# Kernel optimization log

Measured on AMD Instinct MI355X. Metric: run time of the kernel, lower is better.

Reference implementation:

```python
import jax, jax.numpy as jnp
import numpy as np
from jax import lax

C = 256
POOL = 7
NUM_CLASSES = 81
D = NUM_CLASSES - 1
STRIDES = (4, 8, 16, 32)
DEC_MULT = (0.1, 0.1, 0.2, 0.2)  # decode_settings: multipliers on raw deltas
LOG_MAX = float(np.log(1000.0 / 16.0))


def setup_inputs() -> dict:
    key = jax.random.key(0)
    ks = jax.random.split(key, 16)
    n, Rp = 2, 512
    R = n * Rp
    img = 800.0
    cx = jax.random.uniform(ks[0], (R,), minval=0.0, maxval=img)
    cy = jax.random.uniform(ks[1], (R,), minval=0.0, maxval=img)
    w = jax.random.uniform(ks[2], (R,), minval=16.0, maxval=300.0)
    h = jax.random.uniform(ks[3], (R,), minval=16.0, maxval=300.0)
    x1 = jnp.clip(cx - w / 2, 0.0, img - 1.0)
    y1 = jnp.clip(cy - h / 2, 0.0, img - 1.0)
    x2 = jnp.minimum(jnp.maximum(cx + w / 2, x1 + 1.0), img)
    y2 = jnp.minimum(jnp.maximum(cy + h / 2, y1 + 1.0), img)
    proposals = jnp.stack([x1, y1, x2, y2], -1)
    imidx = jnp.repeat(jnp.arange(n, dtype=jnp.int32), Rp)
    fmaps = {}
    for li, s in enumerate(STRIDES):
        hw = int(800 // s)
        fmaps[f"fmap{li}"] = jax.random.normal(ks[4 + li], (n, hw, hw, C), jnp.float32)
    c1, clin = C * POOL * POOL, 1024
    def lin(k, fi, fo):
        return (jax.random.normal(k, (fi, fo), jnp.float32) / np.sqrt(fi).astype(np.float32),
                jnp.zeros((fo,), jnp.float32))
    W0, b0 = lin(ks[8], c1, clin)
    W1, b1 = lin(ks[9], clin, clin)
    Wc, bc = lin(ks[10], clin, NUM_CLASSES)
    Wr, br = lin(ks[11], clin, NUM_CLASSES * 4)
    imsizes = jnp.full((n, 2), img, jnp.float32)  # (h, w) per image
    return dict(proposals=proposals, imidx=imidx, **fmaps,
                W0=W0, b0=b0, W1=W1, b1=b1, Wc=Wc, bc=bc, Wr=Wr, br=br,
                imsizes=imsizes, score_thr=0.05, iou_thr=0.5, imtop=100, min_size=1.0)


def _roi_align_level(fmap, boxes, imidx, stride):
    # fmap [n,H,W,C], boxes [R,4] xyxy in image coords; 1 sample per bin, bilinear.
    n, H, W, c = fmap.shape
    s = 1.0 / stride
    x1, y1, x2, y2 = boxes[:, 0] * s, boxes[:, 1] * s, boxes[:, 2] * s, boxes[:, 3] * s
    g = (jnp.arange(POOL, dtype=jnp.float32) + 0.5) / POOL  # bin centers in [0,1]
    xs = x1[:, None] + g[None, :] * (x2 - x1)[:, None] - 0.5  # [R,POOL]
    ys = y1[:, None] + g[None, :] * (y2 - y1)[:, None] - 0.5
    R = boxes.shape[0]
    xx = jnp.broadcast_to(xs[:, None, :], (R, POOL, POOL))
    yy = jnp.broadcast_to(ys[:, :, None], (R, POOL, POOL))
    x0f, y0f = jnp.floor(xx), jnp.floor(yy)
    wx, wy = xx - x0f, yy - y0f
    x0 = jnp.clip(x0f.astype(jnp.int32), 0, W - 1)
    x1i = jnp.clip(x0f.astype(jnp.int32) + 1, 0, W - 1)
    y0 = jnp.clip(y0f.astype(jnp.int32), 0, H - 1)
    y1i = jnp.clip(y0f.astype(jnp.int32) + 1, 0, H - 1)
    ii = imidx[:, None, None]
    v00 = fmap[ii, y0, x0]; v01 = fmap[ii, y0, x1i]
    v10 = fmap[ii, y1i, x0]; v11 = fmap[ii, y1i, x1i]  # each [R,POOL,POOL,C]
    wx, wy = wx[..., None], wy[..., None]
    return (v00 * (1 - wx) * (1 - wy) + v01 * wx * (1 - wy)
            + v10 * (1 - wx) * wy + v11 * wx * wy)


def _forward(proposals, imidx, fmaps, W0, b0, W1, b1, Wc, bc, Wr, br,
             imsizes, score_thr, iou_thr, imtop, min_size):
    R = proposals.shape[0]
    pw = proposals[:, 2] - proposals[:, 0]
    ph = proposals[:, 3] - proposals[:, 1]
    # FPN level assignment (torchvision canonical formula)
    lvl = jnp.floor(4.0 + jnp.log2(jnp.sqrt(pw * ph) / 224.0 + 1e-6))
    lvl = jnp.clip(lvl, 2, 5).astype(jnp.int32) - 2
    pooled = jnp.zeros((R, POOL, POOL, C), fmaps[0].dtype)
    for k, (fm, st) in enumerate(zip(fmaps, STRIDES)):
        pk = _roi_align_level(fm, proposals, imidx, st)
        pooled = jnp.where((lvl == k)[:, None, None, None], pk, pooled)
    # two-FC head + cls/reg
    x = pooled.reshape(R, -1)
    x = jax.nn.relu(x @ W0 + b0)
    x = jax.nn.relu(x @ W1 + b1)
    reg = (x @ Wr + br).reshape(R, NUM_CLASSES, 4)[:, 1:]      # [R,D,4]
    scr = jax.nn.softmax(x @ Wc + bc, axis=-1)[:, 1:]          # [R,D]
    cls = jnp.broadcast_to(jnp.arange(1, NUM_CLASSES, dtype=jnp.int32), (R, D))
    # decode boxes (proposal cwh + weighted deltas, log-space clamp)
    cx = (proposals[:, 0] + proposals[:, 2]) * 0.5
    cy = (proposals[:, 1] + proposals[:, 3]) * 0.5
    dx = reg[..., 0] * DEC_MULT[0]
    dy = reg[..., 1] * DEC_MULT[1]
    dw = jnp.minimum(reg[..., 2] * DEC_MULT[2], LOG_MAX)
    dh = jnp.minimum(reg[..., 3] * DEC_MULT[3], LOG_MAX)
    ncx = dx * pw[:, None] + cx[:, None]
    ncy = dy * ph[:, None] + cy[:, None]
    nw = jnp.exp(dw) * pw[:, None]
    nh = jnp.exp(dh) * ph[:, None]
    hb = imsizes[imidx, 0][:, None]
    wb = imsizes[imidx, 1][:, None]
    bx1 = jnp.clip(ncx - nw / 2, 0.0, wb); bx2 = jnp.clip(ncx + nw / 2, 0.0, wb)
    by1 = jnp.clip(ncy - nh / 2, 0.0, hb); by2 = jnp.clip(ncy + nh / 2, 0.0, hb)
    boxes = jnp.stack([bx1, by1, bx2, by2], -1)                # [R,D,4]
    valid = (scr > score_thr) & (bx2 - bx1 >= min_size) & (by2 - by1 >= min_size)
    # flatten roi-class pairs; class-offset boxes = torchvision batched_nms trick
    M = R * D
    boxes_f = boxes.reshape(M, 4)
    scr_f = scr.reshape(M)
    cls_f = cls.reshape(M)
    valid_f = valid.reshape(M)
    imidx_f = jnp.repeat(imidx, D)
    off = cls_f.astype(boxes_f.dtype)[:, None] * (jnp.max(imsizes) + 2.0)
    bo = boxes_f + off
    areas = (bo[:, 2] - bo[:, 0]) * (bo[:, 3] - bo[:, 1])
    def nms(scores0):
        def step(scores, _):
            i = jnp.argmax(scores)
            s = scores[i]
            b = bo[i]
            iw = jnp.clip(jnp.minimum(b[2], bo[:, 2]) - jnp.maximum(b[0], bo[:, 0]), 0.0)
            ih = jnp.clip(jnp.minimum(b[3], bo[:, 3]) - jnp.maximum(b[1], bo[:, 1]), 0.0)
            inter = iw * ih
            iou = inter / (areas[i] + areas - inter + 1e-6)
            scores = jnp.where(iou > iou_thr, -1.0, scores)
            scores = scores.at[i].set(-1.0)
            return scores, (i, s)
        _, (idx, s) = lax.scan(step, scores0, None, length=imtop)
        return idx, s
    n = imsizes.shape[0]
    ob, osc, ocl = [], [], []
    for i in range(n):
        s0 = jnp.where(valid_f & (imidx_f == i), scr_f, -1.0)
        idx, s = nms(s0)
        keep = s > 0.0  # padded slots have score <= 0
        ob.append(jnp.where(keep[:, None], boxes_f[idx], 0.0))
        osc.append(jnp.where(keep, s, 0.0))
        ocl.append(jnp.where(keep, cls_f[idx], -1))
    return jnp.stack(ob), jnp.stack(osc), jnp.stack(ocl)


def reference(proposals, imidx, fmap0, fmap1, fmap2, fmap3, W0, b0, W1, b1,
              Wc, bc, Wr, br, imsizes, score_thr, iou_thr, imtop, min_size):
    return _forward(proposals, imidx, (fmap0, fmap1, fmap2, fmap3), W0, b0, W1,
                    b1, Wc, bc, Wr, br, imsizes, score_thr, iou_thr, int(imtop),
                    min_size)
```

## Files before the change

kernel.cpp:

```cpp
#include <hip/hip_runtime.h>
#include <math.h>

#define CCH 256
#define NPOOL 7
#define NCLS 81
#define DCLS 80
#define NHEAD 512
#define FLOG_MAX 4.1351666f

typedef _Float16 half8 __attribute__((ext_vector_type(8)));
typedef _Float16 half4 __attribute__((ext_vector_type(4)));
typedef float floatx4 __attribute__((ext_vector_type(4)));

__global__ void zero_k(float4* __restrict__ p, int count4)
{
    int i = blockIdx.x * blockDim.x + threadIdx.x;
    if (i < count4) p[i] = make_float4(0.f, 0.f, 0.f, 0.f);
}

__device__ __forceinline__ void roi_setup(
    const float* __restrict__ prop, const int* __restrict__ imidx,
    const float* __restrict__ f0, const float* __restrict__ f1,
    const float* __restrict__ f2, const float* __restrict__ f3,
    int h0, int h1, int h2, int h3, int b,
// ... 173 lines not shown
                            const float* __restrict__ bias,
                            _Float16* __restrict__ outH,
                            _Float16* __restrict__ outL,
                            int total, int CL)
{
    int i = (blockIdx.x * blockDim.x + threadIdx.x) * 4;
    if (i >= total) return;
    int b = i % CL;
    float4 v = *(const float4*)(acc + i);
    float4 bb = *(const float4*)(bias + b);
    const float* pv = (const float*)&v;
    const float* pb = (const float*)&bb;
    half4 h, l;
#pragma unroll
    for (int e = 0; e < 4; ++e) {
        float f = fmaxf(pv[e] + pb[e], 0.0f);
        _Float16 hh = (_Float16)f;
        h[e] = hh;
        l[e] = (_Float16)(f - (float)hh);
    }
    *(half4*)(outH + i) = h;
    *(half4*)(outL + i) = l;
}

__device__ __forceinline__ void dma16(const _Float16* g, _Float16* l)
{
    __builtin_amdgcn_global_load_lds(
        (const __attribute__((address_space(1))) unsigned int*)g,
        (__attribute__((address_space(3))) unsigned int*)l, 16, 0, 0);
}

#define LDKE 32

__global__ __launch_bounds__(256) void gemm_mfma_split_k(
    const _Float16* __restrict__ Ah, const _Float16* __restrict__ Al,
    const _Float16* __restrict__ Bh, const _Float16* __restrict__ Bl,
    float* __restrict__ Cacc, int M, int N, int K, int Kc, int SP)
{
    __shared__ _Float16 sAh[128 * LDKE], sAl[128 * LDKE];
    __shared__ _Float16 sBh[128 * LDKE], sBl[128 * LDKE];

    int bid = blockIdx.x;
    int z = bid % SP;
    int q = bid / SP;
    int NT = N >> 7;
    int nn = q % NT;
    int m = q / NT;
    int m0 = m * 128, n0 = nn * 128;
    int kb = z * Kc;
    int ke = min(K, kb + Kc);

    int t = threadIdx.x;
    int lane = t & 63, w = t >> 6;
    int wr = w >> 1, wc = w & 1;
    int fr = lane & 15;
    int fk = (lane >> 4) * 8;

    int drow = w * 32 + (lane >> 2);
    int dkq = (lane & 3) * 8;
    const _Float16* gAh = Ah + (size_t)(m0 + drow) * K + dkq;
    const _Float16* gAl = Al + (size_t)(m0 + drow) * K + dkq;
    const _Float16* gBh = Bh + (size_t)(n0 + drow) * K + dkq;
    const _Float16* gBl = Bl + (size_t)(n0 + drow) * K + dkq;
    size_t rowskip = (size_t)16 * K;

    _Float16* lAh0 = &sAh[(w * 2 + 0) * 512];
    _Float16* lAh1 = &sAh[(w * 2 + 1) * 512];
    _Float16* lAl0 = &sAl[(w * 2 + 0) * 512];
    _Float16* lAl1 = &sAl[(w * 2 + 1) * 512];
    _Float16* lBh0 = &sBh[(w * 2 + 0) * 512];
    _Float16* lBh1 = &sBh[(w * 2 + 1) * 512];
    _Float16* lBl0 = &sBl[(w * 2 + 0) * 512];
    _Float16* lBl1 = &sBl[(w * 2 + 1) * 512];

    floatx4 acc[4][4] = {};

    for (int k0 = kb; k0 < ke; k0 += 32) {
        dma16(gAh + k0, lAh0);
        dma16(gAh + rowskip + k0, lAh1);
        dma16(gAl + k0, lAl0);
        dma16(gAl + rowskip + k0, lAl1);
        dma16(gBh + k0, lBh0);
        dma16(gBh + rowskip + k0, lBh1);
        dma16(gBl + k0, lBl0);
        dma16(gBl + rowskip + k0, lBl1);
        __syncthreads();

        half8 ah[4], al[4], bh[4], bl[4];
#pragma unroll
        for (int i = 0; i < 4; ++i) {
            int ar = wr * 64 + i * 16 + fr;
            ah[i] = *(const half8*)&sAh[ar * LDKE + fk];
            al[i] = *(const half8*)&sAl[ar * LDKE + fk];
            int bc = wc * 64 + i * 16 + fr;
            bh[i] = *(const half8*)&sBh[bc * LDKE + fk];
            bl[i] = *(const half8*)&sBl[bc * LDKE + fk];
        }
#pragma unroll
        for (int i = 0; i < 4; ++i)
#pragma unroll
            for (int j = 0; j < 4; ++j) {
                acc[i][j] = __builtin_amdgcn_mfma_f32_16x16x32_f16(ah[i], bh[j], acc[i][j], 0, 0, 0);
                acc[i][j] = __builtin_amdgcn_mfma_f32_16x16x32_f16(ah[i], bl[j], acc[i][j], 0, 0, 0);
                acc[i][j] = __builtin_amdgcn_mfma_f32_16x16x32_f16(al[i], bh[j], acc[i][j], 0, 0, 0);
            }
        __syncthreads();
    }

    int rbase = (lane >> 4) * 4;
#pragma unroll
    for (int i = 0; i < 4; ++i)
#pragma unroll
        for (int j = 0; j < 4; ++j) {
            int col = n0 + wc * 64 + j * 16 + fr;
#pragma unroll
            for (int r = 0; r < 4; ++r) {
                int row = m0 + wr * 64 + i * 16 + rbase + r;
                atomicAdd(&Cacc[(size_t)row * N + col], acc[i][j][r]);
            }
        }
}

__global__ __launch_bounds__(256) void gemm_mfma_fused64_k(
    const _Float16* __restrict__ Ah, const _Float16* __restrict__ Al,
    const _Float16* __restrict__ Bh, const _Float16* __restrict__ Bl,
    const float* __restrict__ bias,
    float* __restrict__ Cout,
    _Float16* __restrict__ outH, _Float16* __restrict__ outL,
    int M, int N, int K, int mode)
{
    __shared__ _Float16 sAh[64 * LDKE], sAl[64 * LDKE];
    __shared__ _Float16 sBh[64 * LDKE], sBl[64 * LDKE];

    int m0 = blockIdx.y * 64, n0 = blockIdx.x * 64;
    int t = threadIdx.x;
    int lane = t & 63, w = t >> 6;
    int wr = w >> 1, wc = w & 1;
    int fr = lane & 15;
    int fk = (lane >> 4) * 8;

    int drow = w * 16 + (lane >> 2);
    int dkq = (lane & 3) * 8;
    const _Float16* gAh = Ah + (size_t)(m0 + drow) * K + dkq;
    const _Float16* gAl = Al + (size_t)(m0 + drow) * K + dkq;
    const _Float16* gBh = Bh + (size_t)(n0 + drow) * K + dkq;
    const _Float16* gBl = Bl + (size_t)(n0 + drow) * K + dkq;
    _Float16* lAh = &sAh[w * 512];
    _Float16* lAl = &sAl[w * 512];
    _Float16* lBh = &sBh[w * 512];
    _Float16* lBl = &sBl[w * 512];

    floatx4 acc[2][2] = {};

    for (int k0 = 0; k0 < K; k0 += 32) {
        dma16(gAh + k0, lAh);
        dma16(gAl + k0, lAl);
        dma16(gBh + k0, lBh);
        dma16(gBl + k0, lBl);
        __syncthreads();

        half8 ah[2], av[2], bh[2], bv[2];
#pragma unroll
        for (int i = 0; i < 2; ++i) {
            int ar = wr * 32 + i * 16 + fr;
            ah[i] = *(const half8*)&sAh[ar * LDKE + fk];
            av[i] = *(const half8*)&sAl[ar * LDKE + fk];
            int bc = wc * 32 + i * 16 + fr;
            bh[i] = *(const half8*)&sBh[bc * LDKE + fk];
            bv[i] = *(const half8*)&sBl[bc * LDKE + fk];
        }
#pragma unroll
        for (int i = 0; i < 2; ++i)
#pragma unroll
            for (int j = 0; j < 2; ++j) {
                acc[i][j] = __builtin_amdgcn_mfma_f32_16x16x32_f16(ah[i], bh[j], acc[i][j], 0, 0, 0);
                acc[i][j] = __builtin_amdgcn_mfma_f32_16x16x32_f16(ah[i], bv[j], acc[i][j], 0, 0, 0);
                acc[i][j] = __builtin_amdgcn_mfma_f32_16x16x32_f16(av[i], bh[j], acc[i][j], 0, 0, 0);
            }
        __syncthreads();
    }

    int rbase = (lane >> 4) * 4;
#pragma unroll
    for (int i = 0; i < 2; ++i)
#pragma unroll
        for (int j = 0; j < 2; ++j) {
            int col = n0 + wc * 32 + j * 16 + fr;
#pragma unroll
            for (int r = 0; r < 4; ++r) {
                int row = m0 + wr * 32 + i * 16 + rbase + r;
                float v = acc[i][j][r];
                if (mode == 0) {
                    Cout[(size_t)row * N + col] = v;
                } else {
                    float f = fmaxf(v + bias[col], 0.0f);
                    _Float16 hh = (_Float16)f;
                    outH[(size_t)row * N + col] = hh;
                    outL[(size_t)row * N + col] = (_Float16)(f - (float)hh);
                }
            }
        }
}
// ... 71 lines not shown
            if (col < N) atomicAdd(&Cacc[(size_t)row * N + col], acc[i][j]);
        }
    }
}

__global__ void softmax_k(const float* __restrict__ logits, int ldl,
                          const float* __restrict__ bc,
                          float* __restrict__ scr)
{
    int r = blockIdx.x;
    int t = threadIdx.x;
    const float* row = logits + (size_t)r * ldl;

    float v0 = row[t] + bc[t];
    float v1 = (t + 64 < NCLS) ? (row[t + 64] + bc[t + 64]) : -INFINITY;
    float m = fmaxf(v0, v1);
#pragma unroll
    for (int o = 32; o > 0; o >>= 1) m = fmaxf(m, __shfl_down(m, o));
    m = __shfl(m, 0);

    float e0 = expf(v0 - m);
    float e1 = (t + 64 < NCLS) ? expf(v1 - m) : 0.0f;
    float sum = e0 + e1;
#pragma unroll
    for (int o = 32; o > 0; o >>= 1) sum += __shfl_down(sum, o);
    sum = __shfl(sum, 0);
    float inv = 1.0f / sum;

    if (t >= 1)        scr[(size_t)r * DCLS + (t - 1)]  = e0 * inv;
    if (t + 64 < NCLS) scr[(size_t)r * DCLS + (t + 63)] = e1 * inv;
}

#define NMS_T 1024
__global__ __launch_bounds__(NMS_T) void nms_k(
    const float* __restrict__ scr,
    const float* __restrict__ prop,
    const int* __restrict__ imidx,
    const float* __restrict__ head, int ldh, int regofs,
    const float* __restrict__ br,
    const float* __restrict__ imsz,
    const float* __restrict__ score_thr_p,
    const float* __restrict__ min_size_p,
    const float* __restrict__ iou_thr_p,
    int* __restrict__ cidx,
    float* __restrict__ cscore,
    float* __restrict__ cbo,
    float* __restrict__ cbox,
    float* __restrict__ carea,
    float* __restrict__ out,
    int M, int n, int imtop)
{
    int img = blockIdx.x;
    int t = threadIdx.x;
    const int T = NMS_T;

    __shared__ int cnt;
    __shared__ float rs[NMS_T];
    __shared__ int rg[NMS_T];
    __shared__ int rl[NMS_T];
    __shared__ float wb0, wb1, wb2, wb3, wa;

    if (t == 0) cnt = 0;
    __syncthreads();

    float score_thr = score_thr_p[0];
    float min_size  = min_size_p[0];
    float iou_thr   = iou_thr_p[0];
    float immax = imsz[0];
    for (int q = 1; q < 2 * n; ++q) immax = fmaxf(immax, imsz[q]);

    int base = img * M;
    for (int j = t; j < M; j += T) {
        int r = j / DCLS;
        if (imidx[r] != img) continue;
        float s = scr[j];
        if (s <= score_thr) continue;

        int cls = j - r * DCLS + 1;
        const float* pr = prop + (size_t)r * 4;
        float pw = pr[2] - pr[0], ph = pr[3] - pr[1];
        float cx = (pr[0] + pr[2]) * 0.5f, cy = (pr[1] + pr[3]) * 0.5f;
        const float* rg_ = head + (size_t)r * ldh + regofs + cls * 4;
        const float* bb = br + cls * 4;
        float dx = (rg_[0] + bb[0]) * 0.1f;
        float dy = (rg_[1] + bb[1]) * 0.1f;
        float dw = fminf((rg_[2] + bb[2]) * 0.2f, FLOG_MAX);
        float dh = fminf((rg_[3] + bb[3]) * 0.2f, FLOG_MAX);
        float ncx = dx * pw + cx;
        float ncy = dy * ph + cy;
        float nw = expf(dw) * pw;
        float nh = expf(dh) * ph;
        float hbound = imsz[img * 2 + 0];
        float wbound = imsz[img * 2 + 1];
        float bx1 = fminf(fmaxf(ncx - nw * 0.5f, 0.0f), wbound);
        float bx2 = fminf(fmaxf(ncx + nw * 0.5f, 0.0f), wbound);
        float by1 = fminf(fmaxf(ncy - nh * 0.5f, 0.0f), hbound);
        float by2 = fminf(fmaxf(ncy + nh * 0.5f, 0.0f), hbound);
        if (bx2 - bx1 < min_size || by2 - by1 < min_size) continue;

        float off = (float)cls * (immax + 2.0f);
        int p = atomicAdd(&cnt, 1);
        cidx[base + p] = j;
        cscore[base + p] = s;
        cbox[(size_t)(base + p) * 4 + 0] = bx1;
        cbox[(size_t)(base + p) * 4 + 1] = by1;
        cbox[(size_t)(base + p) * 4 + 2] = bx2;
        cbox[(size_t)(base + p) * 4 + 3] = by2;
        cbo[(size_t)(base + p) * 4 + 0] = bx1 + off;
        cbo[(size_t)(base + p) * 4 + 1] = by1 + off;
        cbo[(size_t)(base + p) * 4 + 2] = bx2 + off;
        cbo[(size_t)(base + p) * 4 + 3] = by2 + off;
        carea[base + p] = (bx2 - bx1) * (by2 - by1);
    }
    __syncthreads();
    int K = cnt;

    float* ob  = out;
    float* osc = out + (size_t)n * imtop * 4;
    float* ocl = out + (size_t)n * imtop * 5;

    int it = 0;
    for (; it < imtop; ++it) {
        float best = -1e30f; int bg = 0x7fffffff; int bl = -1;
        for (int p = t; p < K; p += T) {
            float sv = cscore[base + p];
            int g = cidx[base + p];
            if (sv > best || (sv == best && g < bg)) { best = sv; bg = g; bl = p; }
        }
        rs[t] = best; rg[t] = bg; rl[t] = bl;
        __syncthreads();
        for (int o = T / 2; o > 0; o >>= 1) {
            if (t < o) {
                if (rs[t + o] > rs[t] || (rs[t + o] == rs[t] && rg[t + o] < rg[t])) {
                    rs[t] = rs[t + o]; rg[t] = rg[t + o]; rl[t] = rl[t + o];
                }
            }
            __syncthreads();
        }
        float s = rs[0]; int g = rg[0]; int lp = rl[0];
        if (s <= 0.0f) break;

        if (t == 0) {
            size_t oslot = (size_t)img * imtop + it;
            ob[oslot * 4 + 0] = cbox[(size_t)(base + lp) * 4 + 0];
            ob[oslot * 4 + 1] = cbox[(size_t)(base + lp) * 4 + 1];
            ob[oslot * 4 + 2] = cbox[(size_t)(base + lp) * 4 + 2];
            ob[oslot * 4 + 3] = cbox[(size_t)(base + lp) * 4 + 3];
            osc[oslot] = s;
            ocl[oslot] = (float)(g % DCLS + 1);
            wb0 = cbo[(size_t)(base + lp) * 4 + 0];
            wb1 = cbo[(size_t)(base + lp) * 4 + 1];
            wb2 = cbo[(size_t)(base + lp) * 4 + 2];
            wb3 = cbo[(size_t)(base + lp) * 4 + 3];
            wa  = carea[base + lp];
            cscore[base + lp] = -1.0f;
        }
        __syncthreads();
        float b0 = wb0, b1 = wb1, b2 = wb2, b3 = wb3, ai = wa;
        for (int p = t; p < K; p += T) {
            float c0 = cbo[(size_t)(base + p) * 4 + 0];
            float c1 = cbo[(size_t)(base + p) * 4 + 1];
            float c2 = cbo[(size_t)(base + p) * 4 + 2];
            float c3 = cbo[(size_t)(base + p) * 4 + 3];
            float iw = fmaxf(fminf(b2, c2) - fmaxf(b0, c0), 0.0f);
            float ih = fmaxf(fminf(b3, c3) - fmaxf(b1, c1), 0.0f);
            float inter = iw * ih;
            float iou = inter / (ai + carea[base + p] - inter + 1e-6f);
            if (iou > iou_thr) cscore[base + p] = -1.0f;
        }
        __syncthreads();
    }

    for (int q = it + t; q < imtop; q += T) {
        size_t oslot = (size_t)img * imtop + q;
        ob[oslot * 4 + 0] = 0.0f;
        ob[oslot * 4 + 1] = 0.0f;
        ob[oslot * 4 + 2] = 0.0f;
        ob[oslot * 4 + 3] = 0.0f;
        osc[oslot] = 0.0f;
        ocl[oslot] = -1.0f;
    }
}

extern "C" void kernel_launch(void* const* d_in, const int* in_sizes, int n_in,
                              void* d_out, int out_size, void* d_ws, size_t ws_size,
                              hipStream_t stream)
{
    const float* prop   = (const float*)d_in[0];
    const int*   imidx  = (const int*)d_in[1];
    const float* f0     = (const float*)d_in[2];
    const float* f1     = (const float*)d_in[3];
    const float* f2     = (const float*)d_in[4];
    const float* f3     = (const float*)d_in[5];
    const float* W0     = (const float*)d_in[6];
    const float* b0     = (const float*)d_in[7];
    const float* W1     = (const float*)d_in[8];
    const float* b1     = (const float*)d_in[9];
    const float* Wc     = (const float*)d_in[10];
    const float* bc     = (const float*)d_in[11];
    const float* Wr     = (const float*)d_in[12];
    const float* br     = (const float*)d_in[13];
    const float* imsz   = (const float*)d_in[14];
    const float* sthr   = (const float*)d_in[15];
    const float* ithr   = (const float*)d_in[16];
    const float* msz    = (const float*)d_in[18];

    int R = in_sizes[1];
    int n = in_sizes[14] / 2;
    int imtop = out_size / (n * 6);
    int M = R * DCLS;
    int K0 = NPOOL * NPOOL * CCH;
    int CL = in_sizes[7];

    int h0 = (int)(sqrtf((float)(in_sizes[2] / (n * CCH))) + 0.5f);
    int h1 = (int)(sqrtf((float)(in_sizes[3] / (n * CCH))) + 0.5f);
    int h2 = (int)(sqrtf((float)(in_sizes[4] / (n * CCH))) + 0.5f);
    int h3 = (int)(sqrtf((float)(in_sizes[5] / (n * CCH))) + 0.5f);

    float* outf = (float*)d_out;

    size_t szPool  = (size_t)R * K0 * 2;
    size_t szX     = (size_t)R * CL * 4;
    size_t szHead  = (size_t)R * NHEAD * 4;
    size_t szWh    = (size_t)NHEAD * CL * 2;
    size_t szXh    = (size_t)R * CL * 2;
    size_t szW1t   = (size_t)CL * CL * 2;
    size_t szScr   = (size_t)R * DCLS * 4;

    size_t needed = 4 * szPool + 2 * szX + szHead + 2 * szWh
                  + 4 * szXh + 2 * szW1t + szScr;

    int splitK0 = 8;
    bool mfma_ok = (ws_size >= needed) && (R % 128 == 0) && (CL % 128 == 0)
                 && (K0 % (splitK0 * 32) == 0) && (CL % 32 == 0)
                 && ((R * 49) % 4 == 0);

    if (mfma_ok) {
        uint8_t* w = (uint8_t*)d_ws;
        size_t o = 0;
        _Float16* poolH   = (_Float16*)(w + o); o += szPool;
        _Float16* poolL   = (_Float16*)(w + o); o += szPool;
        _Float16* W0tH    = (_Float16*)(w + o); o += szPool;
        _Float16* W0tL    = (_Float16*)(w + o); o += szPool;
        float*    x0acc   = (float*)(w + o);    o += szX;
        float*    unused  = (float*)(w + o);    o += szX;
        float*    headacc = (float*)(w + o);    o += szHead;
        _Float16* WheadtH = (_Float16*)(w + o); o += szWh;
        _Float16* WheadtL = (_Float16*)(w + o); o += szWh;
        _Float16* x0H     = (_Float16*)(w + o); o += szXh;
        _Float16* x0L     = (_Float16*)(w + o); o += szXh;
        _Float16* x1H     = (_Float16*)(w + o); o += szXh;
        _Float16* x1L     = (_Float16*)(w + o); o += szXh;
        _Float16* W1tH    = (_Float16*)(w + o); o += szW1t;
        _Float16* W1tL    = (_Float16*)(w + o); o += szW1t;
        float*    scr     = (float*)(w + o);
        (void)unused;

        int*   cidx   = (int*)d_ws;
        float* cscore = (float*)(cidx + (size_t)n * M);
        float* cbo    = cscore + (size_t)n * M;
        float* cbox   = cbo + (size_t)n * M * 4;
        float* carea  = cbox + (size_t)n * M * 4;

        {
            int c4 = (int)(szX / 16);
            zero_k<<<dim3((c4 + 255) / 256), dim3(256), 0, stream>>>((float4*)x0acc, c4);
        }
        convert_w_t_k<<<dim3(K0 / 64, CL / 64), dim3(256), 0, stream>>>(W0, W0tH, W0tL, K0, CL);
        convert_w_t_k<<<dim3(CL / 64, CL / 64), dim3(256), 0, stream>>>(W1, W1tH, W1tL, CL, CL);
        convert_w_t_guard_k<<<dim3(CL / 64, (NCLS + 63) / 64), dim3(256), 0, stream>>>(
            Wc, WheadtH, WheadtL, CL, NCLS, CL, 0);
        convert_w_t_guard_k<<<dim3(CL / 64, (NCLS * 4 + 63) / 64), dim3(256), 0, stream>>>(
            Wr, WheadtH, WheadtL, CL, NCLS * 4, CL, NCLS);
        roi_align_f16v4_k<<<dim3(R * 49 / 4), dim3(256), 0, stream>>>(
            prop, imidx, f0, f1, f2, f3, h0, h1, h2, h3, poolH, poolL);
        gemm_mfma_split_k<<<dim3(splitK0 * (R / 128) * (CL / 128)), dim3(256), 0, stream>>>(
            poolH, poolL, W0tH, W0tL, x0acc, R, CL, K0, K0 / splitK0, splitK0);
        act_split_k<<<dim3((R * CL / 4 + 255) / 256), dim3(256), 0, stream>>>(
            x0acc, b0, x0H, x0L, R * CL, CL);
        gemm_mfma_fused64_k<<<dim3(CL / 64, R / 64), dim3(256), 0, stream>>>(
            x0H, x0L, W1tH, W1tL, b1, nullptr, x1H, x1L, R, CL, CL, 1);
        gemm_mfma_fused64_k<<<dim3(NHEAD / 64, R / 64), dim3(256), 0, stream>>>(
            x1H, x1L, WheadtH, WheadtL, nullptr, headacc, nullptr, nullptr, R, NHEAD, CL, 0);
        softmax_k<<<dim3(R), dim3(64), 0, stream>>>(headacc, NHEAD, bc, scr);
        nms_k<<<dim3(n), dim3(NMS_T), 0, stream>>>(
            scr, prop, imidx, headacc, NHEAD, NCLS, br, imsz, sthr, msz, ithr,
            cidx, cscore, cbo, cbox, carea, outf, M, n, imtop);
    } else {
        float* ws = (float*)d_ws;
        size_t off = 0;
        float* pooled  = ws + off; off += (size_t)R * K0;
        float* x0acc   = ws + off; off += (size_t)R * CL;
        float* x1acc   = ws + off; off += (size_t)R * CL;
        float* logits  = ws + off; off += (size_t)R * NCLS;
        off = (off + 3) & ~(size_t)3;
        float* reg     = ws + off; off += (size_t)R * NCLS * 4;
        float* scr     = ws + off; off += (size_t)R * DCLS;

        int*   cidx   = (int*)ws;
        float* cscore = (float*)(cidx + (size_t)n * M);
        float* cbo    = cscore + (size_t)n * M;
        float* cbox   = cbo + (size_t)n * M * 4;
        float* carea  = cbox + (size_t)n * M * 4;

        {
            size_t zcount = (size_t)(reg + (size_t)R * NCLS * 4 - x0acc);
            int c4 = (int)(zcount / 4);
            zero_k<<<dim3((c4 + 255) / 256), dim3(256), 0, stream>>>((float4*)x0acc, c4);
        }
        roi_align_k<<<dim3(R * 49), dim3(256), 0, stream>>>(
// ... 16 lines not shown
```

Measured before the change: 429.2 us.

## Use 256x256 double-buffered split-K GEMM with 512 threads and warp-shuffle NMS argmax

Replaces the 128x128 split-K fp16-split MFMA GEMM for the first FC layer with a 256x256 tile kernel using 8 waves and double-buffered LDS filled by global_load_lds. The A and B loads for the next k-step are interleaved between MFMA phases, with setprio and barriers. Split-K changes from 8 to 14. This aims to raise reuse per loaded byte and hide memory latency, at the cost of more registers (a 32-fragment accumulator), a large LDS footprint, and more atomics. The NMS argmax reduction is also moved from a shared-memory tree to warp shuffles, which cuts the number of barriers per iteration.

```diff
diff --git a/kernel.cpp b/kernel.cpp
--- a/kernel.cpp
+++ b/kernel.cpp
@@ -229,90 +229,183 @@
 
 #define LDKE 32
 
-__global__ __launch_bounds__(256) void gemm_mfma_split_k(
+__global__ __launch_bounds__(512, 2) void gemm_mfma_split256_k(
     const _Float16* __restrict__ Ah, const _Float16* __restrict__ Al,
     const _Float16* __restrict__ Bh, const _Float16* __restrict__ Bl,
     float* __restrict__ Cacc, int M, int N, int K, int Kc, int SP)
 {
-    __shared__ _Float16 sAh[128 * LDKE], sAl[128 * LDKE];
-    __shared__ _Float16 sBh[128 * LDKE], sBl[128 * LDKE];
+    __shared__ _Float16 lds[2][4][256 * LDKE];
 
     int bid = blockIdx.x;
-    int z = bid % SP;
-    int q = bid / SP;
-    int NT = N >> 7;
-    int nn = q % NT;
-    int m = q / NT;
-    int m0 = m * 128, n0 = nn * 128;
+    int MT = M >> 8, NT = N >> 8;
+    int tiles = MT * NT;
+    int z = bid / tiles;
+    int q = bid - z * tiles;
+    int nn = q % NT, mm = q / NT;
+    int m0 = mm << 8, n0 = nn << 8;
     int kb = z * Kc;
-    int ke = min(K, kb + Kc);
+    int nt = Kc >> 5;
 
     int t = threadIdx.x;
     int lane = t & 63, w = t >> 6;
-    int wr = w >> 1, wc = w & 1;
+    int wr = w >> 2, wc = w & 3;
     int fr = lane & 15;
     int fk = (lane >> 4) * 8;
 
-    int drow = w * 32 + (lane >> 2);
-    int dkq = (lane & 3) * 8;
-    const _Float16* gAh = Ah + (size_t)(m0 + drow) * K + dkq;
-    const _Float16* gAl = Al + (size_t)(m0 + drow) * K + dkq;
-    const _Float16* gBh = Bh + (size_t)(n0 + drow) * K + dkq;
-    const _Float16* gBl = Bl + (size_t)(n0 + drow) * K + dkq;
-    size_t rowskip = (size_t)16 * K;
-
-    _Float16* lAh0 = &sAh[(w * 2 + 0) * 512];
-    _Float16* lAh1 = &sAh[(w * 2 + 1) * 512];
-    _Float16* lAl0 = &sAl[(w * 2 + 0) * 512];
-    _Float16* lAl1 = &sAl[(w * 2 + 1) * 512];
-    _Float16* lBh0 = &sBh[(w * 2 + 0) * 512];
-    _Float16* lBh1 = &sBh[(w * 2 + 1) * 512];
-    _Float16* lBl0 = &sBl[(w * 2 + 0) * 512];
-    _Float16* lBl1 = &sBl[(w * 2 + 1) * 512];
-
-    floatx4 acc[4][4] = {};
-
-    for (int k0 = kb; k0 < ke; k0 += 32) {
-        dma16(gAh + k0, lAh0);
-        dma16(gAh + rowskip + k0, lAh1);
-        dma16(gAl + k0, lAl0);
-        dma16(gAl + rowskip + k0, lAl1);
-        dma16(gBh + k0, lBh0);
-        dma16(gBh + rowskip + k0, lBh1);
-        dma16(gBl + k0, lBl0);
-        dma16(gBl + rowskip + k0, lBl1);
-        __syncthreads();
-
-        half8 ah[4], al[4], bh[4], bl[4];
-#pragma unroll
-        for (int i = 0; i < 4; ++i) {
-            int ar = wr * 64 + i * 16 + fr;
-            ah[i] = *(const half8*)&sAh[ar * LDKE + fk];
-            al[i] = *(const half8*)&sAl[ar * LDKE + fk];
-            int bc = wc * 64 + i * 16 + fr;
-            bh[i] = *(const half8*)&sBh[bc * LDKE + fk];
-            bl[i] = *(const half8*)&sBl[bc * LDKE + fk];
-        }
-#pragma unroll
-        for (int i = 0; i < 4; ++i)
-#pragma unroll
-            for (int j = 0; j < 4; ++j) {
-                acc[i][j] = __builtin_amdgcn_mfma_f32_16x16x32_f16(ah[i], bh[j], acc[i][j], 0, 0, 0);
-                acc[i][j] = __builtin_amdgcn_mfma_f32_16x16x32_f16(ah[i], bl[j], acc[i][j], 0, 0, 0);
-                acc[i][j] = __builtin_amdgcn_mfma_f32_16x16x32_f16(al[i], bh[j], acc[i][j], 0, 0, 0);
-            }
-        __syncthreads();
-    }
+    int srow = t >> 2;
+    int sch = (t & 3) * 8;
+    const _Float16* gAh0 = Ah + (size_t)(m0 + srow) * K + sch;
+    const _Float16* gAl0 = Al + (size_t)(m0 + srow) * K + sch;
+    const _Float16* gBh0 = Bh + (size_t)(n0 + srow) * K + sch;
+    const _Float16* gBl0 = Bl + (size_t)(n0 + srow) * K + sch;
+    size_t rskip = (size_t)128 * K;
+    int d0 = t * 8;
+    int d1 = 4096 + t * 8;
+
+    floatx4 acc[8][4] = {};
+
+#define STAGE_A(b, kh) do { \
+    dma16(gAh0 + (kh), &lds[b][0][d0]); \
+    dma16(gAh0 + rskip + (kh), &lds[b][0][d1]); \
+    dma16(gAl0 + (kh), &lds[b][1][d0]); \
+    dma16(gAl0 + rskip + (kh), &lds[b][1][d1]); } while (0)
+#define STAGE_B(b, kh) do { \
+    dma16(gBh0 + (kh), &lds[b][2][d0]); \
+    dma16(gBh0 + rskip + (kh), &lds[b][2][d1]); \
+    dma16(gBl0 + (kh), &lds[b][3][d0]); \
+    dma16(gBl0 + rskip + (kh), &lds[b][3][d1]); } while (0)
+
+    STAGE_A(0, kb);
+    STAGE_B(0, kb);
+    asm volatile("s_waitcnt vmcnt(0)" ::: "memory");
+    __builtin_amdgcn_s_barrier();
+
+    int abase = wr * 128 + fr;
+    int bbase = wc * 64 + fr;
+
+#pragma unroll 1
+    for (int tt = 0; tt < nt; ++tt) {
+        int c = tt & 1, nb = c ^ 1;
+        bool hasnext = (tt + 1) < nt;
+        int kh = kb + (tt + 1) * 32;
+
+        const _Float16* sAh = lds[c][0];
+        const _Float16* sAl = lds[c][1];
+        const _Float16* sBh = lds[c][2];
+        const _Float16* sBl = lds[c][3];
+
+        half8 bhf[4], blf[4];
+        half8 a0h, a0l, a1h, a1l;
+
+#pragma unroll
+        for (int j = 0; j < 4; ++j) {
+            int bo = (bbase + j * 16) * LDKE + fk;
+            bhf[j] = *(const half8*)&sBh[bo];
+            blf[j] = *(const half8*)&sBl[bo];
+        }
+        {
+            int a0 = (abase + 0 * 16) * LDKE + fk;
+            int a1 = (abase + 1 * 16) * LDKE + fk;
+            a0h = *(const half8*)&sAh[a0]; a0l = *(const half8*)&sAl[a0];
+            a1h = *(const half8*)&sAh[a1]; a1l = *(const half8*)&sAl[a1];
+        }
+        if (hasnext) STAGE_A(nb, kh);
+        __builtin_amdgcn_s_barrier();
+        asm volatile("s_waitcnt lgkmcnt(0)" ::: "memory");
+        __builtin_amdgcn_sched_barrier(0);
+        __builtin_amdgcn_s_setprio(1);
+#pragma unroll
+        for (int j = 0; j < 4; ++j) {
+            acc[0][j] = __builtin_amdgcn_mfma_f32_16x16x32_f16(a0h, bhf[j], acc[0][j], 0, 0, 0);
+            acc[0][j] = __builtin_amdgcn_mfma_f32_16x16x32_f16(a0h, blf[j], acc[0][j], 0, 0, 0);
+            acc[0][j] = __builtin_amdgcn_mfma_f32_16x16x32_f16(a0l, bhf[j], acc[0][j], 0, 0, 0);
+            acc[1][j] = __builtin_amdgcn_mfma_f32_16x16x32_f16(a1h, bhf[j], acc[1][j], 0, 0, 0);
+            acc[1][j] = __builtin_amdgcn_mfma_f32_16x16x32_f16(a1h, blf[j], acc[1][j], 0, 0, 0);
+            acc[1][j] = __builtin_amdgcn_mfma_f32_16x16x32_f16(a1l, bhf[j], acc[1][j], 0, 0, 0);
+        }
+        __builtin_amdgcn_s_setprio(0);
+        __builtin_amdgcn_s_barrier();
+
+        {
+            int a0 = (abase + 2 * 16) * LDKE + fk;
+            int a1 = (abase + 3 * 16) * LDKE + fk;
+            a0h = *(const half8*)&sAh[a0]; a0l = *(const half8*)&sAl[a0];
+            a1h = *(const half8*)&sAh[a1]; a1l = *(const half8*)&sAl[a1];
+        }
+        if (hasnext) STAGE_B(nb, kh);
+        __builtin_amdgcn_s_barrier();
+        asm volatile("s_waitcnt lgkmcnt(0)" ::: "memory");
+        __builtin_amdgcn_sched_barrier(0);
+        __builtin_amdgcn_s_setprio(1);
+#pragma unroll
+        for (int j = 0; j < 4; ++j) {
+            acc[2][j] = __builtin_amdgcn_mfma_f32_16x16x32_f16(a0h, bhf[j], acc[2][j], 0, 0, 0);
+            acc[2][j] = __builtin_amdgcn_mfma_f32_16x16x32_f16(a0h, blf[j], acc[2][j], 0, 0, 0);
+            acc[2][j] = __builtin_amdgcn_mfma_f32_16x16x32_f16(a0l, bhf[j], acc[2][j], 0, 0, 0);
+            acc[3][j] = __builtin_amdgcn_mfma_f32_16x16x32_f16(a1h, bhf[j], acc[3][j], 0, 0, 0);
+            acc[3][j] = __builtin_amdgcn_mfma_f32_16x16x32_f16(a1h, blf[j], acc[3][j], 0, 0, 0);
+            acc[3][j] = __builtin_amdgcn_mfma_f32_16x16x32_f16(a1l, bhf[j], acc[3][j], 0, 0, 0);
+        }
+        __builtin_amdgcn_s_setprio(0);
+        __builtin_amdgcn_s_barrier();
+
+        {
+            int a0 = (abase + 4 * 16) * LDKE + fk;
+            int a1 = (abase + 5 * 16) * LDKE + fk;
+            a0h = *(const half8*)&sAh[a0]; a0l = *(const half8*)&sAl[a0];
+            a1h = *(const half8*)&sAh[a1]; a1l = *(const half8*)&sAl[a1];
+        }
+        __builtin_amdgcn_s_barrier();
+        asm volatile("s_waitcnt lgkmcnt(0)" ::: "memory");
+        __builtin_amdgcn_sched_barrier(0);
+        __builtin_amdgcn_s_setprio(1);
+#pragma unroll
+        for (int j = 0; j < 4; ++j) {
+            acc[4][j] = __builtin_amdgcn_mfma_f32_16x16x32_f16(a0h, bhf[j], acc[4][j], 0, 0, 0);
+            acc[4][j] = __builtin_amdgcn_mfma_f32_16x16x32_f16(a0h, blf[j], acc[4][j], 0, 0, 0);
+            acc[4][j] = __builtin_amdgcn_mfma_f32_16x16x32_f16(a0l, bhf[j], acc[4][j], 0, 0, 0);
+            acc[5][j] = __builtin_amdgcn_mfma_f32_16x16x32_f16(a1h, bhf[j], acc[5][j], 0, 0, 0);
+            acc[5][j] = __builtin_amdgcn_mfma_f32_16x16x32_f16(a1h, blf[j], acc[5][j], 0, 0, 0);
+            acc[5][j] = __builtin_amdgcn_mfma_f32_16x16x32_f16(a1l, bhf[j], acc[5][j], 0, 0, 0);
+        }
+        __builtin_amdgcn_s_setprio(0);
+        __builtin_amdgcn_s_barrier();
+
+        {
+            int a0 = (abase + 6 * 16) * LDKE + fk;
+            int a1 = (abase + 7 * 16) * LDKE + fk;
+            a0h = *(const half8*)&sAh[a0]; a0l = *(const half8*)&sAl[a0];
+            a1h = *(const half8*)&sAh[a1]; a1l = *(const half8*)&sAl[a1];
+        }
+        __builtin_amdgcn_s_barrier();
+        asm volatile("s_waitcnt lgkmcnt(0)" ::: "memory");
+        __builtin_amdgcn_sched_barrier(0);
+        __builtin_amdgcn_s_setprio(1);
+#pragma unroll
+        for (int j = 0; j < 4; ++j) {
+            acc[6][j] = __builtin_amdgcn_mfma_f32_16x16x32_f16(a0h, bhf[j], acc[6][j], 0, 0, 0);
+            acc[6][j] = __builtin_amdgcn_mfma_f32_16x16x32_f16(a0h, blf[j], acc[6][j], 0, 0, 0);
+            acc[6][j] = __builtin_amdgcn_mfma_f32_16x16x32_f16(a0l, bhf[j], acc[6][j], 0, 0, 0);
+            acc[7][j] = __builtin_amdgcn_mfma_f32_16x16x32_f16(a1h, bhf[j], acc[7][j], 0, 0, 0);
+            acc[7][j] = __builtin_amdgcn_mfma_f32_16x16x32_f16(a1h, blf[j], acc[7][j], 0, 0, 0);
+            acc[7][j] = __builtin_amdgcn_mfma_f32_16x16x32_f16(a1l, bhf[j], acc[7][j], 0, 0, 0);
+        }
+        __builtin_amdgcn_s_setprio(0);
+        asm volatile("s_waitcnt vmcnt(0)" ::: "memory");
+        __builtin_amdgcn_s_barrier();
+    }
+#undef STAGE_A
+#undef STAGE_B
 
     int rbase = (lane >> 4) * 4;
 #pragma unroll
-    for (int i = 0; i < 4; ++i)
+    for (int i = 0; i < 8; ++i)
 #pragma unroll
         for (int j = 0; j < 4; ++j) {
             int col = n0 + wc * 64 + j * 16 + fr;
 #pragma unroll
             for (int r = 0; r < 4; ++r) {
-                int row = m0 + wr * 64 + i * 16 + rbase + r;
+                int row = m0 + wr * 128 + i * 16 + rbase + r;
                 atomicAdd(&Cacc[(size_t)row * N + col], acc[i][j][r]);
             }
         }
@@ -523,11 +616,14 @@
     int img = blockIdx.x;
     int t = threadIdx.x;
     const int T = NMS_T;
+    const int NW = NMS_T / 64;
+    int lane = t & 63, wid = t >> 6;
 
     __shared__ int cnt;
-    __shared__ float rs[NMS_T];
-    __shared__ int rg[NMS_T];
-    __shared__ int rl[NMS_T];
+    __shared__ float wbs[NW];
+    __shared__ int wbg[NW];
+    __shared__ int wbl[NW];
+    __shared__ float fS;
     __shared__ float wb0, wb1, wb2, wb3, wa;
 
     if (t == 0) cnt = 0;
@@ -597,42 +693,56 @@
             int g = cidx[base + p];
             if (sv > best || (sv == best && g < bg)) { best = sv; bg = g; bl = p; }
         }
-        rs[t] = best; rg[t] = bg; rl[t] = bl;
+#pragma unroll
+        for (int o = 32; o > 0; o >>= 1) {
+            float os = __shfl_down(best, o);
+            int   og = __shfl_down(bg, o);
+            int   ol = __shfl_down(bl, o);
+            if (os > best || (os == best && og < bg)) { best = os; bg = og; bl = ol; }
+        }
+        if (lane == 0) { wbs[wid] = best; wbg[wid] = bg; wbl[wid] = bl; }
         __syncthreads();
-        for (int o = T / 2; o > 0; o >>= 1) {
-            if (t < o) {
-                if (rs[t + o] > rs[t] || (rs[t + o] == rs[t] && rg[t + o] < rg[t])) {
-                    rs[t] = rs[t + o]; rg[t] = rg[t + o]; rl[t] = rl[t + o];
+        if (wid == 0) {
+            float b2 = (lane < NW) ? wbs[lane] : -1e30f;
+            int   g2 = (lane < NW) ? wbg[lane] : 0x7fffffff;
+            int   l2 = (lane < NW) ? wbl[lane] : -1;
+#pragma unroll
+            for (int o = NW / 2; o > 0; o >>= 1) {
+                float os = __shfl_down(b2, o);
+                int   og = __shfl_down(g2, o);
+                int   ol = __shfl_down(l2, o);
+                if (os > b2 || (os == b2 && og < g2)) { b2 = os; g2 = og; l2 = ol; }
+            }
+            if (lane == 0) {
+                fS = b2;
+                if (b2 > 0.0f) {
+                    int lp = l2;
+                    size_t oslot = (size_t)img * imtop + it;
+                    ob[oslot * 4 + 0] = cbox[(size_t)(base + lp) * 4 + 0];
+                    ob[oslot * 4 + 1] = cbox[(size_t)(base + lp) * 4 + 1];
+                    ob[oslot * 4 + 2] = cbox[(size_t)(base + lp) * 4 + 2];
+                    ob[oslot * 4 + 3] = cbox[(size_t)(base + lp) * 4 + 3];
+                    osc[oslot] = b2;
+                    ocl[oslot] = (float)(g2 % DCLS + 1);
+                    wb0 = cbo[(size_t)(base + lp) * 4 + 0];
+                    wb1 = cbo[(size_t)(base + lp) * 4 + 1];
+                    wb2 = cbo[(size_t)(base + lp) * 4 + 2];
+                    wb3 = cbo[(size_t)(base + lp) * 4 + 3];
+                    wa  = carea[base + lp];
+                    cscore[base + lp] = -1.0f;
                 }
             }
-            __syncthreads();
-        }
-        float s = rs[0]; int g = rg[0]; int lp = rl[0];
-        if (s <= 0.0f) break;
-
-        if (t == 0) {
-            size_t oslot = (size_t)img * imtop + it;
-            ob[oslot * 4 + 0] = cbox[(size_t)(base + lp) * 4 + 0];
-            ob[oslot * 4 + 1] = cbox[(size_t)(base + lp) * 4 + 1];
-            ob[oslot * 4 + 2] = cbox[(size_t)(base + lp) * 4 + 2];
-            ob[oslot * 4 + 3] = cbox[(size_t)(base + lp) * 4 + 3];
-            osc[oslot] = s;
-            ocl[oslot] = (float)(g % DCLS + 1);
-            wb0 = cbo[(size_t)(base + lp) * 4 + 0];
-            wb1 = cbo[(size_t)(base + lp) * 4 + 1];
-            wb2 = cbo[(size_t)(base + lp) * 4 + 2];
-            wb3 = cbo[(size_t)(base + lp) * 4 + 3];
-            wa  = carea[base + lp];
-            cscore[base + lp] = -1.0f;
         }
         __syncthreads();
-        float b0 = wb0, b1 = wb1, b2 = wb2, b3 = wb3, ai = wa;
+        if (fS <= 0.0f) break;
+
+        float b0 = wb0, b1 = wb1, b2_ = wb2, b3 = wb3, ai = wa;
         for (int p = t; p < K; p += T) {
             float c0 = cbo[(size_t)(base + p) * 4 + 0];
             float c1 = cbo[(size_t)(base + p) * 4 + 1];
             float c2 = cbo[(size_t)(base + p) * 4 + 2];
             float c3 = cbo[(size_t)(base + p) * 4 + 3];
-            float iw = fmaxf(fminf(b2, c2) - fmaxf(b0, c0), 0.0f);
+            float iw = fmaxf(fminf(b2_, c2) - fmaxf(b0, c0), 0.0f);
             float ih = fmaxf(fminf(b3, c3) - fmaxf(b1, c1), 0.0f);
             float inter = iw * ih;
             float iou = inter / (ai + carea[base + p] - inter + 1e-6f);
@@ -700,10 +810,9 @@
     size_t needed = 4 * szPool + 2 * szX + szHead + 2 * szWh
                   + 4 * szXh + 2 * szW1t + szScr;
 
-    int splitK0 = 8;
-    bool mfma_ok = (ws_size >= needed) && (R % 128 == 0) && (CL % 128 == 0)
-                 && (K0 % (splitK0 * 32) == 0) && (CL % 32 == 0)
-                 && ((R * 49) % 4 == 0);
+    const int SP0 = 14;
+    bool mfma_ok = (ws_size >= needed) && (R % 256 == 0) && (CL % 256 == 0)
+                 && (K0 % (SP0 * 32) == 0) && ((R * 49) % 4 == 0);
 
     if (mfma_ok) {
         uint8_t* w = (uint8_t*)d_ws;
@@ -744,8 +853,8 @@
             Wr, WheadtH, WheadtL, CL, NCLS * 4, CL, NCLS);
         roi_align_f16v4_k<<<dim3(R * 49 / 4), dim3(256), 0, stream>>>(
             prop, imidx, f0, f1, f2, f3, h0, h1, h2, h3, poolH, poolL);
-        gemm_mfma_split_k<<<dim3(splitK0 * (R / 128) * (CL / 128)), dim3(256), 0, stream>>>(
-            poolH, poolL, W0tH, W0tL, x0acc, R, CL, K0, K0 / splitK0, splitK0);
+        gemm_mfma_split256_k<<<dim3(SP0 * (R / 256) * (CL / 256)), dim3(512), 0, stream>>>(
+            poolH, poolL, W0tH, W0tL, x0acc, R, CL, K0, K0 / SP0, SP0);
         act_split_k<<<dim3((R * CL / 4 + 255) / 256), dim3(256), 0, stream>>>(
             x0acc, b0, x0H, x0L, R * CL, CL);
         gemm_mfma_fused64_k<<<dim3(CL / 64, R / 64), dim3(256), 0, stream>>>(
```

New measurement: 449.4 us. 1.05x slower.

## Double-buffer fused64 GEMM LDS tiles and keep NMS candidates in registers

Applied to the files above, without the earlier changes.

The fused64 GEMM kernel now uses ping-pong shared-memory buffers and issues the DMA for the next K-tile before computing the current one, so global loads can overlap MFMA work. The NMS kernel replaces its 1024-wide shared-memory tree reduction with wave shuffles plus a small cross-wave step. When the candidate count fits, each thread holds up to 8 candidates' scores, boxes and areas in registers, which avoids re-reading global memory on every one of the up to 100 iterations. The cost is doubled LDS use in the GEMM and higher register pressure in NMS, which could lower occupancy.

```diff
diff --git a/kernel.cpp b/kernel.cpp
--- a/kernel.cpp
+++ b/kernel.cpp
@@ -326,8 +326,8 @@
     _Float16* __restrict__ outH, _Float16* __restrict__ outL,
     int M, int N, int K, int mode)
 {
-    __shared__ _Float16 sAh[64 * LDKE], sAl[64 * LDKE];
-    __shared__ _Float16 sBh[64 * LDKE], sBl[64 * LDKE];
+    __shared__ _Float16 sAh[2][64 * LDKE], sAl[2][64 * LDKE];
+    __shared__ _Float16 sBh[2][64 * LDKE], sBl[2][64 * LDKE];
 
     int m0 = blockIdx.y * 64, n0 = blockIdx.x * 64;
     int t = threadIdx.x;
@@ -342,29 +342,37 @@
     const _Float16* gAl = Al + (size_t)(m0 + drow) * K + dkq;
     const _Float16* gBh = Bh + (size_t)(n0 + drow) * K + dkq;
     const _Float16* gBl = Bl + (size_t)(n0 + drow) * K + dkq;
-    _Float16* lAh = &sAh[w * 512];
-    _Float16* lAl = &sAl[w * 512];
-    _Float16* lBh = &sBh[w * 512];
-    _Float16* lBl = &sBl[w * 512];
+    int lofs = w * 512;
+
+    int nt = K >> 5;
+
+    dma16(gAh + 0, &sAh[0][lofs]);
+    dma16(gAl + 0, &sAl[0][lofs]);
+    dma16(gBh + 0, &sBh[0][lofs]);
+    dma16(gBl + 0, &sBl[0][lofs]);
+    __syncthreads();
 
     floatx4 acc[2][2] = {};
 
-    for (int k0 = 0; k0 < K; k0 += 32) {
-        dma16(gAh + k0, lAh);
-        dma16(gAl + k0, lAl);
-        dma16(gBh + k0, lBh);
-        dma16(gBl + k0, lBl);
-        __syncthreads();
+    for (int tt = 0; tt < nt; ++tt) {
+        int c = tt & 1, nb = c ^ 1;
+        if (tt + 1 < nt) {
+            int k1 = (tt + 1) << 5;
+            dma16(gAh + k1, &sAh[nb][lofs]);
+            dma16(gAl + k1, &sAl[nb][lofs]);
+            dma16(gBh + k1, &sBh[nb][lofs]);
+            dma16(gBl + k1, &sBl[nb][lofs]);
+        }
 
         half8 ah[2], av[2], bh[2], bv[2];
 #pragma unroll
         for (int i = 0; i < 2; ++i) {
             int ar = wr * 32 + i * 16 + fr;
-            ah[i] = *(const half8*)&sAh[ar * LDKE + fk];
-            av[i] = *(const half8*)&sAl[ar * LDKE + fk];
+            ah[i] = *(const half8*)&sAh[c][ar * LDKE + fk];
+            av[i] = *(const half8*)&sAl[c][ar * LDKE + fk];
             int bc = wc * 32 + i * 16 + fr;
-            bh[i] = *(const half8*)&sBh[bc * LDKE + fk];
-            bv[i] = *(const half8*)&sBl[bc * LDKE + fk];
+            bh[i] = *(const half8*)&sBh[c][bc * LDKE + fk];
+            bv[i] = *(const half8*)&sBl[c][bc * LDKE + fk];
         }
 #pragma unroll
         for (int i = 0; i < 2; ++i)
@@ -502,6 +510,7 @@
 }
 
 #define NMS_T 1024
+#define NMS_CPT 8
 __global__ __launch_bounds__(NMS_T) void nms_k(
     const float* __restrict__ scr,
     const float* __restrict__ prop,
@@ -523,12 +532,14 @@
     int img = blockIdx.x;
     int t = threadIdx.x;
     const int T = NMS_T;
+    const int NW = NMS_T / 64;
+    int lane = t & 63, wid = t >> 6;
 
     __shared__ int cnt;
-    __shared__ float rs[NMS_T];
-    __shared__ int rg[NMS_T];
-    __shared__ int rl[NMS_T];
-    __shared__ float wb0, wb1, wb2, wb3, wa;
+    __shared__ float ws_sc[NW], ws_o0[NW], ws_o1[NW], ws_o2[NW], ws_o3[NW], ws_ar[NW];
+    __shared__ int ws_g[NW], ws_p[NW];
+    __shared__ float f_sc, f_o0, f_o1, f_o2, f_o3, f_ar;
+    __shared__ int f_g, f_p;
 
     if (t == 0) cnt = 0;
     __syncthreads();
@@ -590,55 +601,171 @@
     float* ocl = out + (size_t)n * imtop * 5;
 
     int it = 0;
-    for (; it < imtop; ++it) {
-        float best = -1e30f; int bg = 0x7fffffff; int bl = -1;
-        for (int p = t; p < K; p += T) {
-            float sv = cscore[base + p];
-            int g = cidx[base + p];
-            if (sv > best || (sv == best && g < bg)) { best = sv; bg = g; bl = p; }
-        }
-        rs[t] = best; rg[t] = bg; rl[t] = bl;
-        __syncthreads();
-        for (int o = T / 2; o > 0; o >>= 1) {
-            if (t < o) {
-                if (rs[t + o] > rs[t] || (rs[t + o] == rs[t] && rg[t + o] < rg[t])) {
-                    rs[t] = rs[t + o]; rg[t] = rg[t + o]; rl[t] = rl[t + o];
+    if (K <= T * NMS_CPT) {
+        float rsc[NMS_CPT], ro0[NMS_CPT], ro1[NMS_CPT], ro2[NMS_CPT], ro3[NMS_CPT], rar[NMS_CPT];
+        int rgi[NMS_CPT];
+#pragma unroll
+        for (int s = 0; s < NMS_CPT; ++s) {
+            int p = t + s * T;
+            bool ok = p < K;
+            rsc[s] = ok ? cscore[base + p] : -1e30f;
+            rgi[s] = ok ? cidx[base + p] : 0x7fffffff;
+            ro0[s] = ok ? cbo[(size_t)(base + p) * 4 + 0] : 0.0f;
+            ro1[s] = ok ? cbo[(size_t)(base + p) * 4 + 1] : 0.0f;
+            ro2[s] = ok ? cbo[(size_t)(base + p) * 4 + 2] : 0.0f;
+            ro3[s] = ok ? cbo[(size_t)(base + p) * 4 + 3] : 0.0f;
+            rar[s] = ok ? carea[base + p] : 0.0f;
+        }
+
+        for (; it < imtop; ++it) {
+            float bsc = -1e30f; int bg = 0x7fffffff, bp = -1;
+            float b0 = 0.f, b1 = 0.f, b2 = 0.f, b3 = 0.f, ba = 0.f;
+#pragma unroll
+            for (int s = 0; s < NMS_CPT; ++s) {
+                if (rsc[s] > bsc || (rsc[s] == bsc && rgi[s] < bg)) {
+                    bsc = rsc[s]; bg = rgi[s]; bp = t + s * T;
+                    b0 = ro0[s]; b1 = ro1[s]; b2 = ro2[s]; b3 = ro3[s]; ba = rar[s];
                 }
             }
+#pragma unroll
+            for (int o = 32; o > 0; o >>= 1) {
+                float os = __shfl_down(bsc, o);
+                int   og = __shfl_down(bg, o);
+                int   op = __shfl_down(bp, o);
+                float q0 = __shfl_down(b0, o), q1 = __shfl_down(b1, o);
+                float q2 = __shfl_down(b2, o), q3 = __shfl_down(b3, o);
+                float qa = __shfl_down(ba, o);
+                if (os > bsc || (os == bsc && og < bg)) {
+                    bsc = os; bg = og; bp = op;
+                    b0 = q0; b1 = q1; b2 = q2; b3 = q3; ba = qa;
+                }
+            }
+            if (lane == 0) {
+                ws_sc[wid] = bsc; ws_g[wid] = bg; ws_p[wid] = bp;
+                ws_o0[wid] = b0; ws_o1[wid] = b1; ws_o2[wid] = b2; ws_o3[wid] = b3;
+                ws_ar[wid] = ba;
+            }
             __syncthreads();
-        }
-        float s = rs[0]; int g = rg[0]; int lp = rl[0];
-        if (s <= 0.0f) break;
-
-        if (t == 0) {
-            size_t oslot = (size_t)img * imtop + it;
-            ob[oslot * 4 + 0] = cbox[(size_t)(base + lp) * 4 + 0];
-            ob[oslot * 4 + 1] = cbox[(size_t)(base + lp) * 4 + 1];
-            ob[oslot * 4 + 2] = cbox[(size_t)(base + lp) * 4 + 2];
-            ob[oslot * 4 + 3] = cbox[(size_t)(base + lp) * 4 + 3];
-            osc[oslot] = s;
-            ocl[oslot] = (float)(g % DCLS + 1);
-            wb0 = cbo[(size_t)(base + lp) * 4 + 0];
-            wb1 = cbo[(size_t)(base + lp) * 4 + 1];
-            wb2 = cbo[(size_t)(base + lp) * 4 + 2];
-            wb3 = cbo[(size_t)(base + lp) * 4 + 3];
-            wa  = carea[base + lp];
-            cscore[base + lp] = -1.0f;
-        }
-        __syncthreads();
-        float b0 = wb0, b1 = wb1, b2 = wb2, b3 = wb3, ai = wa;
-        for (int p = t; p < K; p += T) {
-            float c0 = cbo[(size_t)(base + p) * 4 + 0];
-            float c1 = cbo[(size_t)(base + p) * 4 + 1];
-            float c2 = cbo[(size_t)(base + p) * 4 + 2];
-            float c3 = cbo[(size_t)(base + p) * 4 + 3];
-            float iw = fmaxf(fminf(b2, c2) - fmaxf(b0, c0), 0.0f);
-            float ih = fmaxf(fminf(b3, c3) - fmaxf(b1, c1), 0.0f);
-            float inter = iw * ih;
-            float iou = inter / (ai + carea[base + p] - inter + 1e-6f);
-            if (iou > iou_thr) cscore[base + p] = -1.0f;
-        }
-        __syncthreads();
+            if (wid == 0) {
+                float s2 = (lane < NW) ? ws_sc[lane] : -1e30f;
+                int   g2 = (lane < NW) ? ws_g[lane] : 0x7fffffff;
+                int   p2 = (lane < NW) ? ws_p[lane] : -1;
+                float c0 = (lane < NW) ? ws_o0[lane] : 0.f;
+                float c1 = (lane < NW) ? ws_o1[lane] : 0.f;
+                float c2 = (lane < NW) ? ws_o2[lane] : 0.f;
+                float c3 = (lane < NW) ? ws_o3[lane] : 0.f;
+                float ca = (lane < NW) ? ws_ar[lane] : 0.f;
+#pragma unroll
+                for (int o = NW / 2; o > 0; o >>= 1) {
+                    float os = __shfl_down(s2, o);
+                    int   og = __shfl_down(g2, o);
+                    int   op = __shfl_down(p2, o);
+                    float q0 = __shfl_down(c0, o), q1 = __shfl_down(c1, o);
+                    float q2 = __shfl_down(c2, o), q3 = __shfl_down(c3, o);
+                    float qa = __shfl_down(ca, o);
+                    if (os > s2 || (os == s2 && og < g2)) {
+                        s2 = os; g2 = og; p2 = op;
+                        c0 = q0; c1 = q1; c2 = q2; c3 = q3; ca = qa;
+                    }
+                }
+                if (lane == 0) {
+                    f_sc = s2; f_g = g2; f_p = p2;
+                    f_o0 = c0; f_o1 = c1; f_o2 = c2; f_o3 = c3; f_ar = ca;
+                }
+            }
+            __syncthreads();
+            float wsc = f_sc;
+            if (wsc <= 0.0f) break;
+            float w0 = f_o0, w1 = f_o1, w2 = f_o2, w3 = f_o3, wa = f_ar;
+            int wp = f_p, wg = f_g;
+
+#pragma unroll
+            for (int s = 0; s < NMS_CPT; ++s) {
+                if (t + s * T == wp) {
+                    size_t oslot = (size_t)img * imtop + it;
+                    ob[oslot * 4 + 0] = cbox[(size_t)(base + wp) * 4 + 0];
+                    ob[oslot * 4 + 1] = cbox[(size_t)(base + wp) * 4 + 1];
+                    ob[oslot * 4 + 2] = cbox[(size_t)(base + wp) * 4 + 2];
+                    ob[oslot * 4 + 3] = cbox[(size_t)(base + wp) * 4 + 3];
+                    osc[oslot] = wsc;
+                    ocl[oslot] = (float)(wg % DCLS + 1);
+                    rsc[s] = -1e30f;
+                }
+            }
+#pragma unroll
+            for (int s = 0; s < NMS_CPT; ++s) {
+                float iw = fmaxf(fminf(w2, ro2[s]) - fmaxf(w0, ro0[s]), 0.0f);
+                float ih = fmaxf(fminf(w3, ro3[s]) - fmaxf(w1, ro1[s]), 0.0f);
+                float inter = iw * ih;
+                float iou = inter / (wa + rar[s] - inter + 1e-6f);
+                if (iou > iou_thr) rsc[s] = -1e30f;
+            }
+        }
+    } else {
+        for (; it < imtop; ++it) {
+            float best = -1e30f; int bg = 0x7fffffff; int bl = -1;
+            for (int p = t; p < K; p += T) {
+                float sv = cscore[base + p];
+                int g = cidx[base + p];
+                if (sv > best || (sv == best && g < bg)) { best = sv; bg = g; bl = p; }
+            }
+#pragma unroll
+            for (int o = 32; o > 0; o >>= 1) {
+                float os = __shfl_down(best, o);
+                int   og = __shfl_down(bg, o);
+                int   ol = __shfl_down(bl, o);
+                if (os > best || (os == best && og < bg)) { best = os; bg = og; bl = ol; }
+            }
+            if (lane == 0) { ws_sc[wid] = best; ws_g[wid] = bg; ws_p[wid] = bl; }
+            __syncthreads();
+            if (wid == 0) {
+                float b2 = (lane < NW) ? ws_sc[lane] : -1e30f;
+                int   g2 = (lane < NW) ? ws_g[lane] : 0x7fffffff;
+                int   l2 = (lane < NW) ? ws_p[lane] : -1;
+#pragma unroll
+                for (int o = NW / 2; o > 0; o >>= 1) {
+                    float os = __shfl_down(b2, o);
+                    int   og = __shfl_down(g2, o);
+                    int   ol = __shfl_down(l2, o);
+                    if (os > b2 || (os == b2 && og < g2)) { b2 = os; g2 = og; l2 = ol; }
+                }
+                if (lane == 0) {
+                    f_sc = b2;
+                    if (b2 > 0.0f) {
+                        int lp = l2;
+                        size_t oslot = (size_t)img * imtop + it;
+                        ob[oslot * 4 + 0] = cbox[(size_t)(base + lp) * 4 + 0];
+                        ob[oslot * 4 + 1] = cbox[(size_t)(base + lp) * 4 + 1];
+                        ob[oslot * 4 + 2] = cbox[(size_t)(base + lp) * 4 + 2];
+                        ob[oslot * 4 + 3] = cbox[(size_t)(base + lp) * 4 + 3];
+                        osc[oslot] = b2;
+                        ocl[oslot] = (float)(g2 % DCLS + 1);
+                        f_o0 = cbo[(size_t)(base + lp) * 4 + 0];
+                        f_o1 = cbo[(size_t)(base + lp) * 4 + 1];
+                        f_o2 = cbo[(size_t)(base + lp) * 4 + 2];
+                        f_o3 = cbo[(size_t)(base + lp) * 4 + 3];
+                        f_ar = carea[base + lp];
+                        cscore[base + lp] = -1.0f;
+                    }
+                }
+            }
+            __syncthreads();
+            if (f_sc <= 0.0f) break;
+
+            float b0 = f_o0, b1 = f_o1, b2_ = f_o2, b3 = f_o3, ai = f_ar;
+            for (int p = t; p < K; p += T) {
+                float c0 = cbo[(size_t)(base + p) * 4 + 0];
+                float c1 = cbo[(size_t)(base + p) * 4 + 1];
+                float c2 = cbo[(size_t)(base + p) * 4 + 2];
+                float c3 = cbo[(size_t)(base + p) * 4 + 3];
+                float iw = fmaxf(fminf(b2_, c2) - fmaxf(b0, c0), 0.0f);
+                float ih = fmaxf(fminf(b3, c3) - fmaxf(b1, c1), 0.0f);
+                float inter = iw * ih;
+                float iou = inter / (ai + carea[base + p] - inter + 1e-6f);
+                if (iou > iou_thr) cscore[base + p] = -1.0f;
+            }
+            __syncthreads();
+        }
     }
 
     for (int q = it + t; q < imtop; q += T) {
```

New measurement: 421.9 us. No clear change (-1.7%).
